# Performance work log

Measured on AMD Instinct MI355X. Metric: run time of the kernel, lower is better.

## Reference

```python
import jax, jax.numpy as jnp
import numpy as np

B, L, D, H = 4, 1024, 512, 8
DK = D // H          # 64
M = 1024             # max_relative_position == L (slicing becomes identity)


def setup_inputs() -> dict:
    key = jax.random.key(0)
    ks = jax.random.split(key, 14)
    s_param = D ** -0.5
    s_rel = DK ** -0.5
    inp = {
        "q": jax.random.normal(ks[0], (B, L, D), jnp.float32),
        "k": jax.random.normal(ks[1], (B, L, D), jnp.float32),
        "v": jax.random.normal(ks[2], (B, L, D), jnp.float32),
        # causal (left-looking) mask, required by the masked rel-pos helper
        "mask": jnp.broadcast_to(jnp.tril(jnp.ones((L, L), jnp.int32)), (B, L, L)),
        # torch nn.Linear params: weight (out,in), bias (out,)
        "wq": jax.random.normal(ks[3], (D, D), jnp.float32) * s_param,
        "bq": jax.random.normal(ks[4], (D,), jnp.float32) * 0.01,
        "wk": jax.random.normal(ks[5], (D, D), jnp.float32) * s_param,
        "bk": jax.random.normal(ks[6], (D,), jnp.float32) * 0.01,
        "wv": jax.random.normal(ks[7], (D, D), jnp.float32) * s_param,
        "bv": jax.random.normal(ks[8], (D,), jnp.float32) * 0.01,
        "wo": jax.random.normal(ks[9], (D, D), jnp.float32) * s_param,
        "bo": jax.random.normal(ks[10], (D,), jnp.float32) * 0.01,
        # relative key embeddings, per-head (heads_share=False): (H, M, DK)
        "rel_k": jax.random.normal(ks[11], (H, M, DK), jnp.float32) * s_rel,
        # time/pitch relative embeddings: (M, M, DK) each
        "rel_time": jax.random.normal(ks[12], (M, M, DK), jnp.float32) * s_rel,
        "rel_pitch": jax.random.normal(ks[13], (M, M, DK), jnp.float32) * s_rel,
    }
    return inp


def _rel_to_abs_masked(x):
    # [B,H,L,L] rel-indexed -> [B,H,L,L] abs-indexed (masked/causal case)
    b, h, l, _ = x.shape
    x = jnp.pad(x, ((0, 0), (0, 0), (0, 0), (1, 0)))
    x = x.reshape(b, h, l + 1, l)
    return x[:, :, 1:, :]


def reference(q, k, v, mask, wq, bq, wk, bk, wv, bv, wo, bo, rel_k, rel_time, rel_pitch):
    b, l, d = q.shape

    def proj(x, w, bias):
        return (x @ w.T + bias).reshape(b, l, H, DK).transpose(0, 2, 1, 3)  # [B,H,L,DK]

    qh = proj(q, wq, bq)
    kh = proj(k, wk, bk)
    vh = proj(v, wv, bv)

    # NOTE: relative branch does NOT scale by 1/sqrt(d_k) (faithful to source)
    logits = jnp.einsum('bhld,bhmd->bhlm', qh, kh)
    logits = jnp.where(mask[:, None, :, :] == 0, -1e9, logits)

    # per-head relative key logits (length == max_rel -> slicing is identity)
    rel_logits = jnp.einsum('bhld,hmd->bhlm', qh, rel_k)
    rel_logits = _rel_to_abs_masked(rel_logits)

    # time + pitch term: torch einsum 'bhld,mmd->bhlm' takes the DIAGONAL of y
    tp_diag = jnp.einsum('mmd->md', rel_time + rel_pitch)  # (M, DK)
    rel_logits = rel_logits + jnp.einsum('bhld,md->bhlm', qh, tp_diag)

    logits = logits + rel_logits
    weights = jax.nn.softmax(logits, axis=-1)
    out = jnp.einsum('bhlm,bhmd->bhld', weights, vh)
    out = out.transpose(0, 2, 1, 3).reshape(b, l, d)
    return out @ wo.T + bo
```

## Files before the change

kernel.cpp:

```cpp
#include <hip/hip_runtime.h>

#define B_ 4
#define L_ 1024
#define D_ 512
#define H_ 8
#define DK_ 64
#define M_ 1024

typedef float f32x4 __attribute__((ext_vector_type(4)));
typedef short bf16x8 __attribute__((ext_vector_type(8)));

#define MFMA16(a, b, c) __builtin_amdgcn_mfma_f32_16x16x32_bf16(a, b, c, 0, 0, 0)
#define SBAR() __builtin_amdgcn_s_barrier()
#define SCHED0() __builtin_amdgcn_sched_barrier(0)

__device__ __forceinline__ ushort bf16_rne(float v) {
    unsigned u = __float_as_uint(v);
    return (ushort)((u + 0x7FFFu + ((u >> 16) & 1u)) >> 16);
}

__device__ __forceinline__ void split8(float4 a, float4 b, bf16x8& hi, bf16x8& lo) {
    unsigned ax = __float_as_uint(a.x), ay = __float_as_uint(a.y);
    unsigned az = __float_as_uint(a.z), aw = __float_as_uint(a.w);
    unsigned bx = __float_as_uint(b.x), by = __float_as_uint(b.y);
    unsigned bz = __float_as_uint(b.z), bw = __float_as_uint(b.w);
    union { unsigned u[4]; bf16x8 v; } H, Lo;
    H.u[0] = (ax >> 16) | (ay & 0xFFFF0000u);
    H.u[1] = (az >> 16) | (aw & 0xFFFF0000u);
    H.u[2] = (bx >> 16) | (by & 0xFFFF0000u);
    H.u[3] = (bz >> 16) | (bw & 0xFFFF0000u);
    float l0 = a.x - __uint_as_float(ax & 0xFFFF0000u);
    float l1 = a.y - __uint_as_float(ay & 0xFFFF0000u);
    float l2 = a.z - __uint_as_float(az & 0xFFFF0000u);
    float l3 = a.w - __uint_as_float(aw & 0xFFFF0000u);
    float l4 = b.x - __uint_as_float(bx & 0xFFFF0000u);
    float l5 = b.y - __uint_as_float(by & 0xFFFF0000u);
    float l6 = b.z - __uint_as_float(bz & 0xFFFF0000u);
    float l7 = b.w - __uint_as_float(bw & 0xFFFF0000u);
    Lo.u[0] = (__float_as_uint(l0) >> 16) | (__float_as_uint(l1) & 0xFFFF0000u);
    Lo.u[1] = (__float_as_uint(l2) >> 16) | (__float_as_uint(l3) & 0xFFFF0000u);
    Lo.u[2] = (__float_as_uint(l4) >> 16) | (__float_as_uint(l5) & 0xFFFF0000u);
    Lo.u[3] = (__float_as_uint(l6) >> 16) | (__float_as_uint(l7) & 0xFFFF0000u);
    hi = H.v;
    lo = Lo.v;
}

__device__ __forceinline__ void gl_lds16(const ushort* g, ushort* l) {
    __builtin_amdgcn_global_load_lds((const __attribute__((address_space(1))) void*)g,
                                     (__attribute__((address_space(3))) void*)l, 16, 0, 0);
}

__device__ __forceinline__ void pack_group(const float* __restrict__ src, int mg,
                                           ushort* __restrict__ hi, ushort* __restrict__ lo,
                                           int tid) {
    const int m_local = tid >> 4;
    const float4* src4 = (const float4*)src;
#pragma unroll
    for (int j = 0; j < 8; ++j) {
        int k4 = (tid & 15) + j * 16;
        float4 val = src4[(size_t)(mg * 16 + m_local) * 128 + k4];
        float vv[4] = {val.x, val.y, val.z, val.w};
        ushort4 h4, l4;
        ushort* hp = (ushort*)&h4;
        ushort* lp = (ushort*)&l4;
#pragma unroll
        for (int e = 0; e < 4; ++e) {
            unsigned u = __float_as_uint(vv[e]);
            hp[e] = (ushort)(u >> 16);
            float lof = vv[e] - __uint_as_float(u & 0xFFFF0000u);
            lp[e] = (ushort)(__float_as_uint(lof) >> 16);
        }
        size_t off = ((size_t)(mg * 16 + (k4 >> 3))) * 512
                     + (((k4 & 7) >> 1) * 16 + m_local) * 8 + (k4 & 1) * 4;
        *(ushort4*)(hi + off) = h4;
        *(ushort4*)(lo + off) = l4;
    }
}

__global__ __launch_bounds__(256) void prep_kernel(
        const float* __restrict__ q, const float* __restrict__ k, const float* __restrict__ v,
        const float* __restrict__ wq, const float* __restrict__ wk,
        const float* __restrict__ wv, const float* __restrict__ wo,
        const float* __restrict__ relk, const float* __restrict__ rt,
        const float* __restrict__ rp,
        ushort* qh, ushort* ql, ushort* kh, ushort* kl, ushort* vh, ushort* vl,
        ushort* wqh, ushort* wql, ushort* wkh, ushort* wkl,
        ushort* wvh, ushort* wvl, ushort* woh, ushort* wol,
        ushort* __restrict__ rpk, float* __restrict__ tp) {
    int bx = blockIdx.x;
    int tid = threadIdx.x;
    if (bx < 768) {
        int w = bx >> 8, mg = bx & 255;
        const float* src = w == 0 ? q : (w == 1 ? k : v);
        ushort* hi = w == 0 ? qh : (w == 1 ? kh : vh);
        ushort* lo = w == 0 ? ql : (w == 1 ? kl : vl);
        pack_group(src, mg, hi, lo, tid);
    } else if (bx < 896) {
        int w = (bx - 768) >> 5, mg = (bx - 768) & 31;
        const float* src = w == 0 ? wq : (w == 1 ? wk : (w == 2 ? wv : wo));
        ushort* hi = w == 0 ? wqh : (w == 1 ? wkh : (w == 2 ? wvh : woh));
        ushort* lo = w == 0 ? wql : (w == 1 ? wkl : (w == 2 ? wvl : wol));
        pack_group(src, mg, hi, lo, tid);
    } else if (bx < 1408) {
        int idx = (bx - 896) * 256 + tid;
        int dk = (idx & 15) * 4;
        int mr = (idx >> 4) & 1023;
        int h  = idx >> 14;
        float4 vv = ((const float4*)relk)[idx];
        ushort4 h4;
        h4.x = bf16_rne(vv.x); h4.y = bf16_rne(vv.y); h4.z = bf16_rne(vv.z); h4.w = bf16_rne(vv.w);
        size_t off = ((((size_t)h * 64 + (mr >> 4)) * 2 + (dk >> 5)) * 64
                      + ((dk >> 3) & 3) * 16 + (mr & 15)) * 8 + (dk & 7);
        *(ushort4*)(rpk + off) = h4;
    } else {
        int idx = (bx - 1408) * 256 + tid;
        int m = idx >> 6;
        size_t off = ((size_t)m * M_ + m) * DK_ + (idx & 63);
        tp[idx] = rt[off] + rp[off];
    }
}

__global__ __launch_bounds__(256) void gemm_qkv(
        const ushort* __restrict__ qsh, const ushort* __restrict__ qsl,
        const ushort* __restrict__ ksh, const ushort* __restrict__ ksl,
        const ushort* __restrict__ vsh, const ushort* __restrict__ vsl,
        const ushort* __restrict__ wqh, const ushort* __restrict__ wql,
        const ushort* __restrict__ wkh, const ushort* __restrict__ wkl,
        const ushort* __restrict__ wvh, const ushort* __restrict__ wvl,
        const float* __restrict__ bq, const float* __restrict__ bk,
        const float* __restrict__ bv, const float* __restrict__ tp,
        ushort* __restrict__ Qhi, ushort* __restrict__ Qlo,
        ushort* __restrict__ Khi, ushort* __restrict__ Klo,
        ushort* __restrict__ Vp) {
    __shared__ __align__(16) ushort st[2][8 * 512];
    __shared__ __align__(16) float pl[4][16 * 68];
    const int z = blockIdx.z;
    const ushort* Ahi = z == 0 ? qsh : z == 1 ? ksh : vsh;
    const ushort* Alo = z == 0 ? qsl : z == 1 ? ksl : vsl;
    const ushort* Bh_ = z == 0 ? wqh : z == 1 ? wkh : wvh;
    const ushort* Bl_ = z == 0 ? wql : z == 1 ? wkl : wvl;
    const float* bias = z == 0 ? bq : z == 1 ? bk : bv;
    ushort* Chi = z == 0 ? Qhi : z == 1 ? Khi : Vp;
    ushort* Clo = z == 0 ? Qlo : Klo;
    const int mode = z + 1;

    const int tid = threadIdx.x;
    const int wv = tid >> 6, l = tid & 63, l8 = l * 8, g = l >> 4, r16 = l & 15;
    const int wm = wv >> 1, wn = wv & 1;
    const int m0 = blockIdx.x * 64;
    const int n0 = blockIdx.y * 128;
    const int n0w = n0 + wn * 64;
    const int ms0 = m0 >> 4, ns0 = n0 >> 4;

    auto stageA = [&](int slot, int kb) {
#pragma unroll
        for (int it = 0; it < 2; ++it) {
            int fid = wv * 2 + it;
            const ushort* src = (fid < 4)
                ? Ahi + ((size_t)(ms0 + fid) * 16 + kb) * 512
                : Alo + ((size_t)(ms0 + fid - 4) * 16 + kb) * 512;
            gl_lds16(src + l8, &st[slot][fid * 512]);
        }
    };

    f32x4 acc[2][4] = {};
    stageA(0, 0);
    for (int kb = 0; kb < 16; ++kb) {
        int cur = kb & 1;
        bf16x8 bfh[4], bfl[4];
#pragma unroll
        for (int t = 0; t < 4; ++t) {
            size_t boff = ((size_t)(ns0 + wn * 4 + t) * 16 + kb) * 512 + l8;
            bfh[t] = *(const bf16x8*)(Bh_ + boff);
            bfl[t] = *(const bf16x8*)(Bl_ + boff);
        }
        if (kb < 15) {
            stageA(cur ^ 1, kb + 1);
            asm volatile("s_waitcnt vmcnt(10)" ::: "memory");
        } else {
            asm volatile("s_waitcnt vmcnt(8)" ::: "memory");
        }
        SCHED0();
        SBAR();
        SCHED0();
        const ushort* S = st[cur];
        bf16x8 ah[2], al_[2];
#pragma unroll
        for (int a = 0; a < 2; ++a) {
            ah[a]  = *(const bf16x8*)(S + (wm * 2 + a) * 512 + l8);
            al_[a] = *(const bf16x8*)(S + (4 + wm * 2 + a) * 512 + l8);
        }
#pragma unroll
        for (int a = 0; a < 2; ++a)
#pragma unroll
            for (int t = 0; t < 4; ++t) {
                acc[a][t] = MFMA16(al_[a], bfh[t], acc[a][t]);
                acc[a][t] = MFMA16(ah[a], bfl[t], acc[a][t]);
                acc[a][t] = MFMA16(ah[a], bfh[t], acc[a][t]);
            }
        SCHED0();
        SBAR();
    }
    float* myp = pl[wv];
    float bv4[4];
#pragma unroll
    for (int t = 0; t < 4; ++t) bv4[t] = bias[n0w + 16 * t + r16];
#pragma unroll
    for (int a = 0; a < 2; ++a)
#pragma unroll
        for (int t = 0; t < 4; ++t)
#pragma unroll
            for (int rg = 0; rg < 4; ++rg) acc[a][t][rg] += bv4[t];

    const int h = n0w >> 6;
#pragma unroll
    for (int a = 0; a < 2; ++a) {
        const int mg = m0 + (wm * 2 + a) * 16;
        const int b = mg >> 10, lrow = mg & 1023;
        const int bh_ = b * 8 + h;
#pragma unroll
        for (int t = 0; t < 4; ++t)
#pragma unroll
            for (int rg = 0; rg < 4; ++rg)
                myp[(4 * g + rg) * 68 + 16 * t + r16] = acc[a][t][rg];
        asm volatile("s_waitcnt lgkmcnt(0)" ::: "memory");
        SCHED0();
        if (mode == 3) {
            if ((g >> 1) == (a & 1)) {
                const int c32 = lrow >> 5;
#pragma unroll
                for (int t2 = 0; t2 < 4; ++t2) {
                    union { ushort u[8]; bf16x8 v8; } pk;
#pragma unroll
                    for (int e = 0; e < 8; ++e)
                        pk.u[e] = bf16_rne(myp[((g & 1) * 8 + e) * 68 + t2 * 16 + r16]);
                    size_t frag = ((size_t)bh_ * 32 + c32) * 4 + t2;
                    *(bf16x8*)(Chi + frag * 512 + l8) = pk.v8;
                }
            }
        } else {
            const int ls = lrow >> 4;
#pragma unroll
            for (int kb2 = 0; kb2 < 2; ++kb2) {
                float4 p0 = *(const float4*)&myp[r16 * 68 + kb2 * 32 + 8 * g];
                float4 p1 = *(const float4*)&myp[r16 * 68 + kb2 * 32 + 8 * g + 4];
                if (mode == 2) {
                    const float* tpp = tp + (size_t)(lrow + r16) * 64 + kb2 * 32 + 8 * g;
                    float4 t0 = *(const float4*)tpp;
                    float4 t1 = *(const float4*)(tpp + 4);
                    p0.x += t0.x; p0.y += t0.y; p0.z += t0.z; p0.w += t0.w;
                    p1.x += t1.x; p1.y += t1.y; p1.z += t1.z; p1.w += t1.w;
                }
                bf16x8 hi8, lo8;
                split8(p0, p1, hi8, lo8);
                size_t frag = ((size_t)bh_ * 64 + ls) * 2 + kb2;
                *(bf16x8*)(Chi + frag * 512 + l8) = hi8;
                *(bf16x8*)(Clo + frag * 512 + l8) = lo8;
            }
        }
    }
}

__device__ const int kPerm[24] = {7,22,23,16,18,19,21,15, 20,6,5,12,14,4,10,17, 0,1,2,3,9,8,11,13};

__global__ __launch_bounds__(256, 3) void attn_mfma(
        const ushort* __restrict__ qhi_g, const ushort* __restrict__ qlo_g,
        const ushort* __restrict__ khi_g, const ushort* __restrict__ klo_g,
        const ushort* __restrict__ vp_g, const ushort* __restrict__ rp_g,
        ushort* __restrict__ ahi, ushort* __restrict__ alo,
        float* __restrict__ po, float* __restrict__ pm, float* __restrict__ pls) {
    __shared__ __align__(16) ushort st[2][16 * 512];
    __shared__ __align__(16) float pl[4][16 * 68];
    const int tid = threadIdx.x;
    const int wv = tid >> 6, l = tid & 63, l8 = l * 8, g = l >> 4, r16 = l & 15;
    const int id = (int)blockIdx.x;
    const int bh = id / 24;
    const int c = kPerm[id - bh * 24];
    int rt, t0, cnt, split, slot;
    if (c < 8) { rt = c; t0 = 0; cnt = c + 1; split = 0; slot = 0; }
    else {
        int j = c - 8;
        rt = 8 + (j >> 1);
        slot = j & 1;
        int ntf = rt + 1, nA = (ntf + 1) >> 1;
        t0 = slot ? nA : 0;
        cnt = slot ? ntf - nA : nA;
        split = 1;
    }
    const int h = bh & (H_ - 1);
    const int i0 = rt * 64 + wv * 16;
    const ushort* khb = khi_g + (size_t)bh * 65536;
    const ushort* klb = klo_g + (size_t)bh * 65536;
    const ushort* vvb = vp_g + (size_t)bh * 65536;
    const ushort* rrb = rp_g + (size_t)h * 65536;
    float* myp = pl[wv];

    bf16x8 qhi[2], qlo[2];
    {
        const size_t qf = ((size_t)bh * 64 + (i0 >> 4)) * 2;
#pragma unroll
        for (int kt = 0; kt < 2; ++kt) {
            qhi[kt] = *(const bf16x8*)(qhi_g + (qf + kt) * 512 + l8);
            qlo[kt] = *(const bf16x8*)(qlo_g + (qf + kt) * 512 + l8);
        }
    }
    f32x4 o[4] = {};
    float m_run[4], l_run[4];
#pragma unroll
    for (int rg = 0; rg < 4; ++rg) { m_run[rg] = -INFINITY; l_run[rg] = 0.f; }

    auto stageK = [&](int sl, int t) {
        const int c8 = t * 8;
#pragma unroll
        for (int it = 0; it < 4; ++it) {
            int fid = wv * 4 + it;
            const ushort* gsrc = (fid < 8) ? khb + ((size_t)(c8 + fid)) * 512
                                           : klb + ((size_t)(c8 + fid - 8)) * 512;
            gl_lds16(gsrc + l8, &st[sl][fid * 512]);
        }
    };

    stageK(0, t0);
    for (int ti = 0; ti < cnt; ++ti) {
        const int t = t0 + ti, c0 = t * 64, cur = ti & 1;
        const int fb = (1008 - i0 + c0) >> 4;
        bf16x8 rh[2][5];
#pragma unroll
        for (int u = 0; u < 5; ++u) {
            int gf = fb + u;
            gf = gf > 63 ? 63 : gf;
#pragma unroll
            for (int kt = 0; kt < 2; ++kt)
                rh[kt][u] = *(const bf16x8*)(rrb + ((size_t)gf * 2 + kt) * 512 + l8);
        }
        bf16x8 vh[2][4];
#pragma unroll
        for (int kt = 0; kt < 2; ++kt)
#pragma unroll
            for (int tt = 0; tt < 4; ++tt)
                vh[kt][tt] = *(const bf16x8*)(vvb + ((size_t)(t * 8 + kt * 4 + tt)) * 512 + l8);
        SCHED0();
        if (ti + 1 < cnt) {
            stageK(cur ^ 1, t + 1);
            asm volatile("s_waitcnt vmcnt(22)" ::: "memory");
        } else {
            asm volatile("s_waitcnt vmcnt(18)" ::: "memory");
        }
        SCHED0();
        SBAR();
        SCHED0();
        const ushort* sb = st[cur];

        f32x4 s[4] = {};
        f32x4 rr[5] = {};
#pragma unroll
        for (int kt = 0; kt < 2; ++kt) {
#pragma unroll
            for (int tt = 0; tt < 4; ++tt) {
                bf16x8 kh8 = *(const bf16x8*)(sb + (tt * 2 + kt) * 512 + l8);
                bf16x8 kl8 = *(const bf16x8*)(sb + (8 + tt * 2 + kt) * 512 + l8);
                s[tt] = MFMA16(qlo[kt], kh8, s[tt]);
                s[tt] = MFMA16(qhi[kt], kl8, s[tt]);
                s[tt] = MFMA16(qhi[kt], kh8, s[tt]);
            }
#pragma unroll
            for (int u = 0; u < 5; ++u) {
                rr[u] = MFMA16(qhi[kt], rh[kt][u], rr[u]);
                rr[u] = MFMA16(qlo[kt], rh[kt][u], rr[u]);
            }
        }
#pragma unroll
        for (int rg = 0; rg < 4; ++rg) {
            int d = r16 + 15 - 4 * g - rg;
            int lp = (l & 48) | (d & 15);
            bool hi_sel = d >= 16;
#pragma unroll
            for (int tt = 0; tt < 4; ++tt) {
                float va = __shfl(rr[tt][rg], lp);
                float vb = __shfl(rr[tt + 1][rg], lp);
                s[tt][rg] += hi_sel ? vb : va;
            }
        }
        if (c0 + 63 > i0) {
#pragma unroll
            for (int tt = 0; tt < 4; ++tt)
#pragma unroll
                for (int rg = 0; rg < 4; ++rg)
                    if (c0 + 16 * tt + r16 > i0 + 4 * g + rg) s[tt][rg] = -INFINITY;
        }
#pragma unroll
        for (int rg = 0; rg < 4; ++rg) {
            float mx = fmaxf(fmaxf(s[0][rg], s[1][rg]), fmaxf(s[2][rg], s[3][rg]));
#pragma unroll
            for (int off = 1; off < 16; off <<= 1) mx = fmaxf(mx, __shfl_xor(mx, off));
            float mnew = fmaxf(m_run[rg], mx);
            float sc = __expf(m_run[rg] - mnew);
            float sum = 0.f;
#pragma unroll
            for (int tt = 0; tt < 4; ++tt) {
                float p = __expf(s[tt][rg] - mnew);
                s[tt][rg] = p;
                sum += p;
            }
#pragma unroll
            for (int off = 1; off < 16; off <<= 1) sum += __shfl_xor(sum, off);
            l_run[rg] = l_run[rg] * sc + sum;
            m_run[rg] = mnew;
#pragma unroll
            for (int tt = 0; tt < 4; ++tt) o[tt][rg] *= sc;
        }
#pragma unroll
        for (int tt = 0; tt < 4; ++tt)
#pragma unroll
            for (int rg = 0; rg < 4; ++rg)
                myp[(4 * g + rg) * 68 + 16 * tt + r16] = s[tt][rg];
        asm volatile("s_waitcnt lgkmcnt(0)" ::: "memory");
#pragma unroll
        for (int kt = 0; kt < 2; ++kt) {
            const float* pp = myp + r16 * 68 + kt * 32 + g * 8;
            bf16x8 phi, plo;
            split8(*(const float4*)pp, *(const float4*)(pp + 4), phi, plo);
#pragma unroll
            for (int tt = 0; tt < 4; ++tt) {
                o[tt] = MFMA16(plo, vh[kt][tt], o[tt]);
                o[tt] = MFMA16(phi, vh[kt][tt], o[tt]);
            }
        }
        SCHED0();
        SBAR();
    }
    if (!split) {
#pragma unroll
        for (int tt = 0; tt < 4; ++tt)
#pragma unroll
            for (int rg = 0; rg < 4; ++rg)
                myp[(4 * g + rg) * 68 + 16 * tt + r16] = o[tt][rg] / l_run[rg];
        asm volatile("s_waitcnt lgkmcnt(0)" ::: "memory");
        SCHED0();
        const size_t mstripG = (size_t)(bh >> 3) * 64 + (i0 >> 4);
#pragma unroll
        for (int kb = 0; kb < 2; ++kb) {
            float4 p0 = *(const float4*)&myp[r16 * 68 + kb * 32 + 8 * g];
            float4 p1 = *(const float4*)&myp[r16 * 68 + kb * 32 + 8 * g + 4];
            bf16x8 hi8, lo8;
            split8(p0, p1, hi8, lo8);
            size_t frag = mstripG * 16 + ((bh & 7) * 2 + kb);
            *(bf16x8*)(ahi + frag * 512 + l8) = hi8;
            *(bf16x8*)(alo + frag * 512 + l8) = lo8;
        }
    } else {
        const int gi2 = (bh * 8 + (rt - 8)) * 2 + slot;
        float* poB = po + (size_t)gi2 * 4096;
#pragma unroll
        for (int tt = 0; tt < 4; ++tt)
#pragma unroll
            for (int rg = 0; rg < 4; ++rg)
                poB[(wv * 16 + 4 * g + rg) * 64 + 16 * tt + r16] = o[tt][rg];
        if (r16 == 0) {
#pragma unroll
            for (int rg = 0; rg < 4; ++rg) {
                int row = wv * 16 + 4 * g + rg;
                pm[gi2 * 64 + row] = m_run[rg];
                pls[gi2 * 64 + row] = l_run[rg];
            }
        }
    }
}

__global__ __launch_bounds__(256) void combine_kernel(
        const float* __restrict__ po, const float* __restrict__ pm,
        const float* __restrict__ pls,
        ushort* __restrict__ ahi, ushort* __restrict__ alo) {
    const int gi = blockIdx.x;
    const int bh = gi >> 3, rt = 8 + (gi & 7);
    const int tid = threadIdx.x;
    const int wv = tid >> 6, l = tid & 63, l8 = l * 8, g = l >> 4, r16 = l & 15;
    const int row = wv * 16 + r16;
    float mA = pm[(gi * 2 + 0) * 64 + row], mB = pm[(gi * 2 + 1) * 64 + row];
    float lA = pls[(gi * 2 + 0) * 64 + row], lB = pls[(gi * 2 + 1) * 64 + row];
    float m = fmaxf(mA, mB);
    float eA = __expf(mA - m), eB = __expf(mB - m);
    float inv = 1.0f / (lA * eA + lB * eB);
    eA *= inv; eB *= inv;
    const float* poA = po + (size_t)(gi * 2 + 0) * 4096 + row * 64;
    const float* poB = po + (size_t)(gi * 2 + 1) * 4096 + row * 64;
    const size_t mstripG = (size_t)(bh >> 3) * 64 + rt * 4 + wv;
#pragma unroll
    for (int kb = 0; kb < 2; ++kb) {
        int dk0 = kb * 32 + g * 8;
        float4 a0 = *(const float4*)(poA + dk0);
        float4 a1 = *(const float4*)(poA + dk0 + 4);
        float4 b0 = *(const float4*)(poB + dk0);
        float4 b1 = *(const float4*)(poB + dk0 + 4);
        float4 p0, p1;
        p0.x = a0.x * eA + b0.x * eB; p0.y = a0.y * eA + b0.y * eB;
        p0.z = a0.z * eA + b0.z * eB; p0.w = a0.w * eA + b0.w * eB;
        p1.x = a1.x * eA + b1.x * eB; p1.y = a1.y * eA + b1.y * eB;
        p1.z = a1.z * eA + b1.z * eB; p1.w = a1.w * eA + b1.w * eB;
        bf16x8 hi8, lo8;
        split8(p0, p1, hi8, lo8);
        size_t frag = mstripG * 16 + ((bh & 7) * 2 + kb);
        *(bf16x8*)(ahi + frag * 512 + l8) = hi8;
        *(bf16x8*)(alo + frag * 512 + l8) = lo8;
    }
}

__global__ __launch_bounds__(256) void gemm_out(
        const ushort* __restrict__ Ahi, const ushort* __restrict__ Alo,
        const ushort* __restrict__ Bh_, const ushort* __restrict__ Bl_,
        const float* __restrict__ bias, float* __restrict__ Cf) {
    __shared__ __align__(16) ushort st[2][16 * 512];
    const int tid = threadIdx.x;
    const int wv = tid >> 6, l = tid & 63, l8 = l * 8, g = l >> 4, r16 = l & 15;
    const int m0 = blockIdx.x * 64;
    const int n0 = blockIdx.y * 64;
    const int ms0 = m0 >> 4, ns0 = n0 >> 4;

    auto stageA2 = [&](int slot, int kbp) {
#pragma unroll
        for (int it = 0; it < 4; ++it) {
            int fid = wv * 4 + it;
            int hf  = fid >> 3;
            int sb_ = fid & 7;
            int kb  = kbp * 2 + hf;
            const ushort* src = (sb_ < 4)
                ? Ahi + ((size_t)(ms0 + sb_) * 16 + kb) * 512
                : Alo + ((size_t)(ms0 + sb_ - 4) * 16 + kb) * 512;
            gl_lds16(src + l8, &st[slot][fid * 512]);
        }
    };

    f32x4 acc[4] = {};
    stageA2(0, 0);
    for (int kbp = 0; kbp < 8; ++kbp) {
        int cur = kbp & 1;
        bf16x8 bfh[2][4], bfl[2][4];
#pragma unroll
        for (int hf = 0; hf < 2; ++hf)
#pragma unroll
            for (int t = 0; t < 4; ++t) {
                size_t boff = ((size_t)(ns0 + t) * 16 + kbp * 2 + hf) * 512 + l8;
                bfh[hf][t] = *(const bf16x8*)(Bh_ + boff);
                bfl[hf][t] = *(const bf16x8*)(Bl_ + boff);
            }
        if (kbp < 7) {
            stageA2(cur ^ 1, kbp + 1);
            asm volatile("s_waitcnt vmcnt(20)" ::: "memory");
        } else {
            asm volatile("s_waitcnt vmcnt(16)" ::: "memory");
        }
        SCHED0();
        SBAR();
        SCHED0();
        const ushort* S = st[cur];
#pragma unroll
        for (int hf = 0; hf < 2; ++hf) {
            bf16x8 ah  = *(const bf16x8*)(S + (hf * 8 + wv) * 512 + l8);
            bf16x8 al_ = *(const bf16x8*)(S + (hf * 8 + 4 + wv) * 512 + l8);
#pragma unroll
            for (int t = 0; t < 4; ++t) {
                acc[t] = MFMA16(al_, bfh[hf][t], acc[t]);
                acc[t] = MFMA16(ah, bfl[hf][t], acc[t]);
                acc[t] = MFMA16(ah, bfh[hf][t], acc[t]);
            }
        }
        SCHED0();
        SBAR();
    }
#pragma unroll
    for (int t = 0; t < 4; ++t) {
        float bvv = bias[n0 + 16 * t + r16];
#pragma unroll
        for (int rg = 0; rg < 4; ++rg)
            Cf[(size_t)(m0 + wv * 16 + 4 * g + rg) * 512 + n0 + 16 * t + r16] = acc[t][rg] + bvv;
    }
}

extern "C" void kernel_launch(void* const* d_in, const int* in_sizes, int n_in,
                              void* d_out, int out_size, void* d_ws, size_t ws_size,
                              hipStream_t stream) {
    const float* q    = (const float*)d_in[0];
    const float* k    = (const float*)d_in[1];
    const float* v    = (const float*)d_in[2];
    const float* wq   = (const float*)d_in[4];
    const float* bq   = (const float*)d_in[5];
    const float* wk   = (const float*)d_in[6];
    const float* bk   = (const float*)d_in[7];
    const float* wv   = (const float*)d_in[8];
    const float* bv   = (const float*)d_in[9];
    const float* wo   = (const float*)d_in[10];
    const float* bo   = (const float*)d_in[11];
    const float* relk = (const float*)d_in[12];
    const float* rt   = (const float*)d_in[13];
    const float* rp   = (const float*)d_in[14];
    float* out = (float*)d_out;

    const size_t NE = (size_t)B_ * H_ * L_ * DK_;
    const size_t WE = (size_t)D_ * D_;
    char* p = (char*)d_ws;
    float* tp    = (float*)p;      p += (size_t)M_ * DK_ * 4;
    ushort* rpk  = (ushort*)p;     p += (size_t)H_ * M_ * DK_ * 2;
    ushort* qsh  = (ushort*)p;     p += NE * 2;
    ushort* qsl  = (ushort*)p;     p += NE * 2;
    ushort* ksh  = (ushort*)p;     p += NE * 2;
    ushort* ksl  = (ushort*)p;     p += NE * 2;
    ushort* vsh  = (ushort*)p;     p += NE * 2;
    ushort* vsl  = (ushort*)p;     p += NE * 2;
    ushort* wqh  = (ushort*)p;     p += WE * 2;
    ushort* wql  = (ushort*)p;     p += WE * 2;
    ushort* wkh  = (ushort*)p;     p += WE * 2;
    ushort* wkl  = (ushort*)p;     p += WE * 2;
    ushort* wvh  = (ushort*)p;     p += WE * 2;
    ushort* wvl  = (ushort*)p;     p += WE * 2;
    ushort* woh  = (ushort*)p;     p += WE * 2;
    ushort* wol  = (ushort*)p;     p += WE * 2;
    ushort* Qhi  = (ushort*)p;     p += NE * 2;
    ushort* Qlo  = (ushort*)p;     p += NE * 2;
    ushort* Khi  = (ushort*)p;     p += NE * 2;
    ushort* Klo  = (ushort*)p;     p += NE * 2;
    ushort* Vp   = (ushort*)p;     p += NE * 2;
    ushort* Ah2  = (ushort*)p;     p += NE * 2;
    ushort* Al2  = (ushort*)p;     p += NE * 2;
    float* po    = (float*)p;      p += (size_t)512 * 4096 * 4;
    float* pm    = (float*)p;      p += (size_t)512 * 64 * 4;
    float* pls   = (float*)p;      p += (size_t)512 * 64 * 4;

    prep_kernel<<<dim3(1664), 256, 0, stream>>>(q, k, v, wq, wk, wv, wo, relk, rt, rp,
                                                qsh, qsl, ksh, ksl, vsh, vsl,
                                                wqh, wql, wkh, wkl, wvh, wvl, woh, wol,
                                                rpk, tp);

    gemm_qkv<<<dim3(B_ * L_ / 64, D_ / 128, 3), 256, 0, stream>>>(
        qsh, qsl, ksh, ksl, vsh, vsl, wqh, wql, wkh, wkl, wvh, wvl,
        bq, bk, bv, tp, Qhi, Qlo, Khi, Klo, Vp);

    attn_mfma<<<dim3(768), 256, 0, stream>>>(Qhi, Qlo, Khi, Klo, Vp, rpk, Ah2, Al2,
                                             po, pm, pls);

    combine_kernel<<<dim3(256), 256, 0, stream>>>(po, pm, pls, Ah2, Al2);

    gemm_out<<<dim3(B_ * L_ / 64, D_ / 64), 256, 0, stream>>>(Ah2, Al2, woh, wol, bo, out);
}
```

Baseline: 98.23 us.

## Replace LDS-staged A tiles with register double-buffered direct global loads in GEMMs

In the QKV projection and output projection GEMMs, the A operand no longer goes through shared memory with async global-to-LDS copies and block barriers. Each wave now loads its own A and B fragments straight into registers, ping-ponging between two register sets so the next k-step's loads overlap the current MFMAs. This removes LDS traffic and the two barriers per k-step, at the cost of higher register pressure. A fragments that several waves share are now fetched once per wave from global/L2 instead of once per block.

New measurement: 98.08 us. About the same (-0.2%).

```diff
diff --git a/kernel.cpp b/kernel.cpp
--- a/kernel.cpp
+++ b/kernel.cpp
@@ -132,7 +132,6 @@
         ushort* __restrict__ Qhi, ushort* __restrict__ Qlo,
         ushort* __restrict__ Khi, ushort* __restrict__ Klo,
         ushort* __restrict__ Vp) {
-    __shared__ __align__(16) ushort st[2][8 * 512];
     __shared__ __align__(16) float pl[4][16 * 68];
     const int z = blockIdx.z;
     const ushort* Ahi = z == 0 ? qsh : z == 1 ? ksh : vsh;
@@ -152,54 +151,53 @@
     const int n0w = n0 + wn * 64;
     const int ms0 = m0 >> 4, ns0 = n0 >> 4;
 
-    auto stageA = [&](int slot, int kb) {
-#pragma unroll
-        for (int it = 0; it < 2; ++it) {
-            int fid = wv * 2 + it;
-            const ushort* src = (fid < 4)
-                ? Ahi + ((size_t)(ms0 + fid) * 16 + kb) * 512
-                : Alo + ((size_t)(ms0 + fid - 4) * 16 + kb) * 512;
-            gl_lds16(src + l8, &st[slot][fid * 512]);
+    auto loadA = [&](int kb, bf16x8* ah, bf16x8* al) {
+#pragma unroll
+        for (int a = 0; a < 2; ++a) {
+            size_t aoff = ((size_t)(ms0 + wm * 2 + a) * 16 + kb) * 512 + l8;
+            ah[a] = *(const bf16x8*)(Ahi + aoff);
+            al[a] = *(const bf16x8*)(Alo + aoff);
         }
     };
-
-    f32x4 acc[2][4] = {};
-    stageA(0, 0);
-    for (int kb = 0; kb < 16; ++kb) {
-        int cur = kb & 1;
-        bf16x8 bfh[4], bfl[4];
+    auto loadB = [&](int kb, bf16x8* bh, bf16x8* bl) {
 #pragma unroll
         for (int t = 0; t < 4; ++t) {
             size_t boff = ((size_t)(ns0 + wn * 4 + t) * 16 + kb) * 512 + l8;
-            bfh[t] = *(const bf16x8*)(Bh_ + boff);
-            bfl[t] = *(const bf16x8*)(Bl_ + boff);
-        }
-        if (kb < 15) {
-            stageA(cur ^ 1, kb + 1);
-            asm volatile("s_waitcnt vmcnt(10)" ::: "memory");
-        } else {
-            asm volatile("s_waitcnt vmcnt(8)" ::: "memory");
-        }
-        SCHED0();
-        SBAR();
-        SCHED0();
-        const ushort* S = st[cur];
-        bf16x8 ah[2], al_[2];
-#pragma unroll
-        for (int a = 0; a < 2; ++a) {
-            ah[a]  = *(const bf16x8*)(S + (wm * 2 + a) * 512 + l8);
-            al_[a] = *(const bf16x8*)(S + (4 + wm * 2 + a) * 512 + l8);
-        }
+            bh[t] = *(const bf16x8*)(Bh_ + boff);
+            bl[t] = *(const bf16x8*)(Bl_ + boff);
+        }
+    };
+
+    f32x4 acc[2][4] = {};
+    bf16x8 ah0[2], al0[2], bh0[4], bl0[4];
+    bf16x8 ah1[2], al1[2], bh1[4], bl1[4];
+    loadA(0, ah0, al0);
+    loadB(0, bh0, bl0);
+#pragma unroll 1
+    for (int kb2 = 0; kb2 < 8; ++kb2) {
+        const int kb = kb2 * 2;
+        loadA(kb + 1, ah1, al1);
+        loadB(kb + 1, bh1, bl1);
 #pragma unroll
         for (int a = 0; a < 2; ++a)
 #pragma unroll
             for (int t = 0; t < 4; ++t) {
-                acc[a][t] = MFMA16(al_[a], bfh[t], acc[a][t]);
-                acc[a][t] = MFMA16(ah[a], bfl[t], acc[a][t]);
-                acc[a][t] = MFMA16(ah[a], bfh[t], acc[a][t]);
-            }
-        SCHED0();
-        SBAR();
+                acc[a][t] = MFMA16(al0[a], bh0[t], acc[a][t]);
+                acc[a][t] = MFMA16(ah0[a], bl0[t], acc[a][t]);
+                acc[a][t] = MFMA16(ah0[a], bh0[t], acc[a][t]);
+            }
+        if (kb + 2 < 16) {
+            loadA(kb + 2, ah0, al0);
+            loadB(kb + 2, bh0, bl0);
+        }
+#pragma unroll
+        for (int a = 0; a < 2; ++a)
+#pragma unroll
+            for (int t = 0; t < 4; ++t) {
+                acc[a][t] = MFMA16(al1[a], bh1[t], acc[a][t]);
+                acc[a][t] = MFMA16(ah1[a], bl1[t], acc[a][t]);
+                acc[a][t] = MFMA16(ah1[a], bh1[t], acc[a][t]);
+            }
     }
     float* myp = pl[wv];
     float bv4[4];
@@ -509,63 +507,52 @@
         const ushort* __restrict__ Ahi, const ushort* __restrict__ Alo,
         const ushort* __restrict__ Bh_, const ushort* __restrict__ Bl_,
         const float* __restrict__ bias, float* __restrict__ Cf) {
-    __shared__ __align__(16) ushort st[2][16 * 512];
     const int tid = threadIdx.x;
     const int wv = tid >> 6, l = tid & 63, l8 = l * 8, g = l >> 4, r16 = l & 15;
     const int m0 = blockIdx.x * 64;
     const int n0 = blockIdx.y * 64;
     const int ms0 = m0 >> 4, ns0 = n0 >> 4;
 
-    auto stageA2 = [&](int slot, int kbp) {
-#pragma unroll
-        for (int it = 0; it < 4; ++it) {
-            int fid = wv * 4 + it;
-            int hf  = fid >> 3;
-            int sb_ = fid & 7;
-            int kb  = kbp * 2 + hf;
-            const ushort* src = (sb_ < 4)
-                ? Ahi + ((size_t)(ms0 + sb_) * 16 + kb) * 512
-                : Alo + ((size_t)(ms0 + sb_ - 4) * 16 + kb) * 512;
-            gl_lds16(src + l8, &st[slot][fid * 512]);
-        }
+    auto loadA = [&](int kb, bf16x8& ah, bf16x8& al) {
+        size_t aoff = ((size_t)(ms0 + wv) * 16 + kb) * 512 + l8;
+        ah = *(const bf16x8*)(Ahi + aoff);
+        al = *(const bf16x8*)(Alo + aoff);
     };
+    auto loadB = [&](int kb, bf16x8* bh, bf16x8* bl) {
+#pragma unroll
+        for (int t = 0; t < 4; ++t) {
+            size_t boff = ((size_t)(ns0 + t) * 16 + kb) * 512 + l8;
+            bh[t] = *(const bf16x8*)(Bh_ + boff);
+            bl[t] = *(const bf16x8*)(Bl_ + boff);
+        }
+    };
 
     f32x4 acc[4] = {};
-    stageA2(0, 0);
-    for (int kbp = 0; kbp < 8; ++kbp) {
-        int cur = kbp & 1;
-        bf16x8 bfh[2][4], bfl[2][4];
-#pragma unroll
-        for (int hf = 0; hf < 2; ++hf)
-#pragma unroll
-            for (int t = 0; t < 4; ++t) {
-                size_t boff = ((size_t)(ns0 + t) * 16 + kbp * 2 + hf) * 512 + l8;
-                bfh[hf][t] = *(const bf16x8*)(Bh_ + boff);
-                bfl[hf][t] = *(const bf16x8*)(Bl_ + boff);
-            }
-        if (kbp < 7) {
-            stageA2(cur ^ 1, kbp + 1);
-            asm volatile("s_waitcnt vmcnt(20)" ::: "memory");
-        } else {
-            asm volatile("s_waitcnt vmcnt(16)" ::: "memory");
-        }
-        SCHED0();
-        SBAR();
-        SCHED0();
-        const ushort* S = st[cur];
-#pragma unroll
-        for (int hf = 0; hf < 2; ++hf) {
-            bf16x8 ah  = *(const bf16x8*)(S + (hf * 8 + wv) * 512 + l8);
-            bf16x8 al_ = *(const bf16x8*)(S + (hf * 8 + 4 + wv) * 512 + l8);
-#pragma unroll
-            for (int t = 0; t < 4; ++t) {
-                acc[t] = MFMA16(al_, bfh[hf][t], acc[t]);
-                acc[t] = MFMA16(ah, bfl[hf][t], acc[t]);
-                acc[t] = MFMA16(ah, bfh[hf][t], acc[t]);
-            }
-        }
-        SCHED0();
-        SBAR();
+    bf16x8 ah0, al0, bh0[4], bl0[4];
+    bf16x8 ah1, al1, bh1[4], bl1[4];
+    loadA(0, ah0, al0);
+    loadB(0, bh0, bl0);
+#pragma unroll 1
+    for (int kb2 = 0; kb2 < 8; ++kb2) {
+        const int kb = kb2 * 2;
+        loadA(kb + 1, ah1, al1);
+        loadB(kb + 1, bh1, bl1);
+#pragma unroll
+        for (int t = 0; t < 4; ++t) {
+            acc[t] = MFMA16(al0, bh0[t], acc[t]);
+            acc[t] = MFMA16(ah0, bl0[t], acc[t]);
+            acc[t] = MFMA16(ah0, bh0[t], acc[t]);
+        }
+        if (kb + 2 < 16) {
+            loadA(kb + 2, ah0, al0);
+            loadB(kb + 2, bh0, bl0);
+        }
+#pragma unroll
+        for (int t = 0; t < 4; ++t) {
+            acc[t] = MFMA16(al1, bh1[t], acc[t]);
+            acc[t] = MFMA16(ah1, bl1[t], acc[t]);
+            acc[t] = MFMA16(ah1, bh1[t], acc[t]);
+        }
     }
 #pragma unroll
     for (int t = 0; t < 4; ++t) {
```
